# Kernel optimization log

Hardware: AMD Instinct MI355X
Metric: run time of the kernel (lower is better)

Reference implementation:

```python
import jax, jax.numpy as jnp
import numpy as np

B, C, H, W, L, R = 1, 32, 96, 128, 2, 3
N = 2 * R + 1
EPS = 1e-5


def conv2d(x, w, stride=1, pad=1):
    return jax.lax.conv_general_dilated(
        x, w, (stride, stride), ((pad, pad), (pad, pad)),
        dimension_numbers=('NCHW', 'OIHW', 'NCHW'))


def conv_transpose2d(x, w, stride=2, pad=1):
    # torch ConvTranspose2d semantics; w: [Cin, Cout, kH, kW]
    kh, kw = w.shape[2], w.shape[3]
    wf = jnp.flip(w, (2, 3)).transpose(1, 0, 2, 3)  # [Cout, Cin, kh, kw]
    return jax.lax.conv_general_dilated(
        x, wf, (1, 1),
        ((kh - 1 - pad, kh - 1 - pad), (kw - 1 - pad, kw - 1 - pad)),
        lhs_dilation=(stride, stride),
        dimension_numbers=('NCHW', 'OIHW', 'NCHW'))


def bnorm(x, s, b, m, v):
    # inference-mode BatchNorm2d (fixed running stats)
    inv = s * jax.lax.rsqrt(v + EPS)
    return x * inv[None, :, None, None] + (b - m * inv)[None, :, None, None]


def grid_sample(img, grid):
    # bilinear, align_corners=True, padding_mode='zeros'
    # img [B,C,H,W], grid [B,Hg,Wg,2] (x,y) in [-1,1]
    Bi, Ci, Hi, Wi = img.shape
    gx = (grid[..., 0] + 1.0) * 0.5 * (Wi - 1)
    gy = (grid[..., 1] + 1.0) * 0.5 * (Hi - 1)
    x0 = jnp.floor(gx)
    y0 = jnp.floor(gy)
    wx = (gx - x0)[:, None]  # [B,1,Hg,Wg]
    wy = (gy - y0)[:, None]

    def tap(yf, xf):
        valid = (xf >= 0) & (xf <= Wi - 1) & (yf >= 0) & (yf <= Hi - 1)
        xc = jnp.clip(xf, 0, Wi - 1).astype(jnp.int32)
        yc = jnp.clip(yf, 0, Hi - 1).astype(jnp.int32)
        v = jax.vmap(lambda im, y, x: im[:, y, x])(img, yc, xc)  # [B,C,Hg,Wg]
        return v * valid[:, None].astype(img.dtype)

    v00 = tap(y0, x0)
    v01 = tap(y0, x0 + 1)
    v10 = tap(y0 + 1, x0)
    v11 = tap(y0 + 1, x0 + 1)
    return (v00 * (1 - wx) * (1 - wy) + v01 * wx * (1 - wy)
            + v10 * (1 - wx) * wy + v11 * wx * wy)


def _forward(fmap1_0, fmap1_1, fmap2_0, fmap2_1, coords,
             cw1, cw2, cw3, cw4, ctw5, cw6, cb6,
             bn1s, bn1b, bn1m, bn1v, bn2s, bn2b, bn2m, bn2v,
             bn3s, bn3b, bn3m, bn3v, bn4s, bn4b, bn4m, bn4v,
             bn5s, bn5b, bn5m, bn5v, dap_w):
    n = N
    dx = jnp.linspace(-R, R, n)
    delta = jnp.stack(jnp.meshgrid(dx, dx, indexing='ij'), axis=-1)  # [n,n,2]
    b, _, h, w = coords.shape
    cp = coords.transpose(0, 2, 3, 1)  # [b,h,w,2] (x,y)
    bns = ((bn1s, bn1b, bn1m, bn1v), (bn2s, bn2b, bn2m, bn2v),
           (bn3s, bn3b, bn3m, bn3v), (bn4s, bn4b, bn4m, bn4v),
           (bn5s, bn5b, bn5m, bn5v))
    out = []
    for i, (f1, f2) in enumerate(((fmap1_0, fmap2_0), (fmap1_1, fmap2_1))):
        c, h2, w2 = f1.shape[1], f1.shape[2], f1.shape[3]
        # [b,n,h,n,w,2]: first n axis pairs with h, second with w (as in torch view)
        cent = cp[:, None, :, None, :, :] / (2.0 ** i) + delta[None, :, None, :, None, :]
        gx = 2.0 * cent[..., 0] / (w2 - 1) - 1.0
        gy = 2.0 * cent[..., 1] / (h2 - 1) - 1.0
        grid = jnp.stack([gx, gy], -1).reshape(b, n * h, n * w, 2)
        f2s = grid_sample(f2, grid).reshape(b, c, n, h, n, w)
        f2s = f2s.transpose(0, 2, 4, 1, 3, 5)  # [b,du,dv,c,h,w]
        f1e = jnp.broadcast_to(f1[:, None, None], (b, n, n, c, h, w))
        x = jnp.concatenate([f1e, f2s], axis=3).reshape(b * n * n, 2 * c, h, w)
        # MatchingNet (DICL): conv-bn-relu stack, stride-2 down + transposed up
        x = jax.nn.relu(bnorm(conv2d(x, cw1[i]), *(p[i] for p in bns[0])))
        x = jax.nn.relu(bnorm(conv2d(x, cw2[i], stride=2), *(p[i] for p in bns[1])))
        x = jax.nn.relu(bnorm(conv2d(x, cw3[i]), *(p[i] for p in bns[2])))
        x = jax.nn.relu(bnorm(conv2d(x, cw4[i]), *(p[i] for p in bns[3])))
        x = jax.nn.relu(bnorm(conv_transpose2d(x, ctw5[i]), *(p[i] for p in bns[4])))
        x = conv2d(x, cw6[i]) + cb6[i][None, :, None, None]  # [b*n*n,1,h,w]
        cost = x.reshape(b, n * n, h, w)
        # DisplacementAwareProjection: 1x1 conv over the 49 displacement channels
        cost = jnp.einsum('pq,bqhw->bphw', dap_w[i], cost)
        out.append(cost)
    return jnp.concatenate(out, axis=1)  # [b, L*(2r+1)^2, h, w]


def setup_inputs():
    key = jax.random.key(0)
    ks = jax.random.split(key, 40)

    def rn(k, shape, scale=1.0):
        return jax.random.normal(k, shape, jnp.float32) * scale

    inp = {}
    inp['fmap1_0'] = rn(ks[0], (B, C, H, W))
    inp['fmap2_0'] = rn(ks[1], (B, C, H, W))
    inp['fmap1_1'] = rn(ks[2], (B, C, H, W))
    inp['fmap2_1'] = rn(ks[3], (B, C, H, W))
    gy, gx = jnp.meshgrid(jnp.arange(H, dtype=jnp.float32),
                          jnp.arange(W, dtype=jnp.float32), indexing='ij')
    base = jnp.stack([gx, gy], 0)[None]  # [1,2,H,W] (x,y) pixel coords
    inp['coords'] = base + rn(ks[4], (B, 2, H, W), 2.0)

    def cw(k, co, ci, kk):
        return rn(k, (L, co, ci, kk, kk), 1.0 / np.sqrt(ci * kk * kk))

    inp['cw1'] = cw(ks[5], 96, 2 * C, 3)
    inp['cw2'] = cw(ks[6], 128, 96, 3)
    inp['cw3'] = cw(ks[7], 128, 128, 3)
    inp['cw4'] = cw(ks[8], 64, 128, 3)
    inp['ctw5'] = rn(ks[9], (L, 64, 32, 4, 4), 1.0 / np.sqrt(64 * 16))
    inp['cw6'] = cw(ks[10], 1, 32, 3)
    inp['cb6'] = rn(ks[11], (L, 1), 0.1)
    for j, ch in enumerate((96, 128, 128, 64, 32), start=1):
        k4 = jax.random.split(ks[11 + j], 4)
        inp['bn%ds' % j] = 1.0 + rn(k4[0], (L, ch), 0.1)
        inp['bn%db' % j] = rn(k4[1], (L, ch), 0.1)
        inp['bn%dm' % j] = rn(k4[2], (L, ch), 0.1)
        inp['bn%dv' % j] = 1.0 + rn(k4[3], (L, ch), 0.1) ** 2
    # DAP identity init
    inp['dap_w'] = jnp.tile(jnp.eye(N * N, dtype=jnp.float32)[None], (L, 1, 1))
    return inp


def reference(fmap1_0, fmap1_1, fmap2_0, fmap2_1, coords,
              cw1, cw2, cw3, cw4, ctw5, cw6, cb6,
              bn1s, bn1b, bn1m, bn1v, bn2s, bn2b, bn2m, bn2v,
              bn3s, bn3b, bn3m, bn3v, bn4s, bn4b, bn4m, bn4v,
              bn5s, bn5b, bn5m, bn5v, dap_w):
    return _forward(fmap1_0, fmap1_1, fmap2_0, fmap2_1, coords,
                    cw1, cw2, cw3, cw4, ctw5, cw6, cb6,
                    bn1s, bn1b, bn1m, bn1v, bn2s, bn2b, bn2m, bn2v,
                    bn3s, bn3b, bn3m, bn3v, bn4s, bn4b, bn4m, bn4v,
                    bn5s, bn5b, bn5m, bn5v, dap_w)
```

## Files before the change

### kernel.cpp

```cpp
#include <hip/hip_runtime.h>

#define EPSF 1e-5f

typedef __attribute__((ext_vector_type(8))) short short8;
typedef __attribute__((ext_vector_type(4))) float f32x4;

__device__ __forceinline__ ushort f2bf(float x) {
    union { float f; unsigned u; } c; c.f = x;
    unsigned r = c.u + 0x7FFF + ((c.u >> 16) & 1);
    return (ushort)(r >> 16);
}
__device__ __forceinline__ float bf2f(ushort b) {
    union { unsigned u; float f; } c; c.u = ((unsigned)b) << 16;
    return c.f;
}
__device__ __forceinline__ int swz(int a) {
    return a ^ (((a >> 7) & 7) << 4);
}


__global__ __launch_bounds__(256) void k_repack_conv(
    const float* __restrict__ src, ushort* __restrict__ dst, int CO, int CI)
{
    int idx = blockIdx.x * 256 + threadIdx.x;
    if (idx >= CO * CI * 9) return;
    int co = idx / (CI * 9);
    int rem = idx % (CI * 9);
    int ci = rem / 9, tap = rem % 9;
    dst[((size_t)tap * CO + co) * CI + ci] = f2bf(src[idx]);
}

__global__ __launch_bounds__(256) void k_repack_ct(
    const float* __restrict__ src, ushort* __restrict__ dst)
{
    int idx = blockIdx.x * 256 + threadIdx.x;
    if (idx >= 4 * 4 * 32 * 64) return;
    int ci = idx & 63;
    int t = idx >> 6;
    int co = t & 31; t >>= 5;
    int tap = t & 3;
    int parity = t >> 2;
    int ph = parity >> 1, pw = parity & 1;
    int a = tap >> 1, b = tap & 1;
    int kh = ((ph + 1) & 1) + 2 * a;
    int kw = ((pw + 1) & 1) + 2 * b;
    dst[idx] = f2bf(src[((ci * 32 + co) * 4 + kh) * 4 + kw]);
}

__global__ __launch_bounds__(256) void k_pack_f1(
    const float* __restrict__ f1_0, const float* __restrict__ f1_1,
    ushort* __restrict__ xf1)
{
    const int sp = blockIdx.x * 256 + threadIdx.x;
    const int l = blockIdx.z;
    const float* f1 = l ? f1_1 : f1_0;
    ushort* dst = xf1 + (size_t)l * 393216 + (size_t)sp * 32;
    #pragma unroll
    for (int g = 0; g < 4; ++g) {
        uint4 pk;
        uint* pw_ = (uint*)&pk;
        #pragma unroll
        for (int q = 0; q < 4; ++q) {
            int c = g * 8 + q * 2;
            pw_[q] = (uint)f2bf(f1[(size_t)c * 12288 + sp])
                   | ((uint)f2bf(f1[(size_t)(c + 1) * 12288 + sp]) << 16);
        }
        *(uint4*)(dst + g * 8) = pk;
    }
}

__global__ __launch_bounds__(256) void k_sample_nhwc(
    const float* __restrict__ f2_0, const float* __restrict__ f2_1,
    const float* __restrict__ coords, ushort* __restrict__ x0s, int d0)
{
    const int HW = 12288;
    const int sp = blockIdx.x * 256 + threadIdx.x;
    const int slot = blockIdx.z;
    const int p = d0 + slot;
    const int l = p / 49;
    const int d = p - l * 49;
    const int du = d / 7, dv = d % 7;
    const float inv_scale = l ? 0.5f : 1.0f;
    const float* f2 = l ? f2_1 : f2_0;

    float cx = coords[sp] * inv_scale + (float)(du - 3);
    float cy = coords[HW + sp] * inv_scale + (float)(dv - 3);
    float xf = floorf(cx), yf = floorf(cy);
    float wx = cx - xf, wy = cy - yf;
    int xi = (int)xf, yi = (int)yf;
    float vx0 = (xf >= 0.f && xf <= 127.f) ? 1.f : 0.f;
    float vx1 = (xf + 1.f >= 0.f && xf + 1.f <= 127.f) ? 1.f : 0.f;
    float vy0 = (yf >= 0.f && yf <= 95.f) ? 1.f : 0.f;
    float vy1 = (yf + 1.f >= 0.f && yf + 1.f <= 95.f) ? 1.f : 0.f;
    int x0i = min(max(xi, 0), 127), x1i = min(max(xi + 1, 0), 127);
    int y0i = min(max(yi, 0), 95),  y1i = min(max(yi + 1, 0), 95);
    float w00 = (1.f - wx) * (1.f - wy) * vx0 * vy0;
    float w01 = wx * (1.f - wy) * vx1 * vy0;
    float w10 = (1.f - wx) * wy * vx0 * vy1;
    float w11 = wx * wy * vx1 * vy1;
    int o00 = y0i * 128 + x0i, o01 = y0i * 128 + x1i;
    int o10 = y1i * 128 + x0i, o11 = y1i * 128 + x1i;

    ushort* dst = x0s + ((size_t)slot * HW + sp) * 32;
    #pragma unroll
    for (int g = 0; g < 4; ++g) {
        uint4 pk;
        uint* pw_ = (uint*)&pk;
        #pragma unroll
        for (int q = 0; q < 4; ++q) {
            uint wv = 0;
            #pragma unroll
            for (int h = 0; h < 2; ++h) {
                int c = g * 8 + q * 2 + h;
                const float* fc = f2 + (size_t)c * HW;
                float s = w00 * fc[o00] + w01 * fc[o01] + w10 * fc[o10] + w11 * fc[o11];
                wv |= ((uint)f2bf(s)) << (16 * h);
            }
            pw_[q] = wv;
        }
        *(uint4*)(dst + g * 8) = pk;
    }
}

template <int EPI>
__global__ __launch_bounds__(512, 2) void k_conv1(
    const ushort* __restrict__ in,
    ushort* __restrict__ out,
    const ushort* __restrict__ wbase,
    const float* __restrict__ p1,
    const float* __restrict__ bs0, const float* __restrict__ bb0,
    const float* __restrict__ bm0, const float* __restrict__ bv0,
    int d0, int koff)
{
    constexpr int AB = 10 * 66 * 64;
    constexpr int PB = 3 * 48 * 64;
    constexpr int SA = 6;
    __shared__ __align__(16) char smem[AB + 2 * PB];
    char* As = smem;

    const int tid = threadIdx.x;
    const int lane = tid & 63, wid = tid >> 6;
    const int lr = lane & 15, kg = lane >> 4;
    const int bx = blockIdx.x;
    const int rt = bx >> 1, ct = bx & 1;
    const int r0 = rt * 8, c0 = ct * 64;
    const int y = blockIdx.y;
    const int co0 = y * 48;
    const int slot = blockIdx.z;
    const int l = EPI ? slot : (d0 + slot) / 49;

    const ushort* ib = in + (size_t)slot * 12288 * 32;
    const ushort* wl = wbase + (size_t)l * (9 * 96 * 64);
    const short8 z8 = {0, 0, 0, 0, 0, 0, 0, 0};

    #pragma unroll
    for (int i = 0; i < SA; ++i) {
        int lin = i * 8192 + tid * 16;
        if (lin < AB) {
            int pos = lin >> 6;
            int prow = (pos * 994) >> 16;
            int pcol = pos - prow * 66;
            int grow = r0 - 1 + prow, gcol = c0 - 1 + pcol;
            bool ok = ((unsigned)grow < 96u) && ((unsigned)gcol < 128u);
            short8 v = z8;
            if (ok) v = *(const short8*)(ib + (grow * 128 + gcol) * 32 + ((lin & 63) >> 1));
            *(short8*)(As + swz(lin)) = v;
        }
    }

    int boff[2]; unsigned bmask = 0;
    #pragma unroll
    for (int i = 0; i < 2; ++i) {
        int lin = i * 8192 + tid * 16;
        if (lin < PB) bmask |= 1u << i;
        int lc = min(lin, PB - 16);
        int rowidx = lc >> 6;
        int tpg = rowidx / 48;
        int r = rowidx - tpg * 48;
        boff[i] = (tpg * 96 + co0 + r) * 64 + koff + ((lc & 63) >> 1);
    }
    short8 stgB[2];
    auto loadB = [&](int pg) {
        const ushort* src = wl + pg * (3 * 96 * 64);
        #pragma unroll
        for (int i = 0; i < 2; ++i)
            if ((bmask >> i) & 1) stgB[i] = *(const short8*)(src + boff[i]);
    };
    auto writeB = [&](int pg) {
        char* Bs = smem + AB + (pg & 1) * PB;
        #pragma unroll
        for (int i = 0; i < 2; ++i) {
            int lin = i * 8192 + tid * 16;
            if ((bmask >> i) & 1) *(short8*)(Bs + swz(lin)) = stgB[i];
        }
    };

    f32x4 acc[4][3];
    if constexpr (EPI == 0) {
        const float* pl = p1 + (size_t)l * 1179648
                        + ((size_t)((bx * 2 + y) * 512 + tid)) * 48;
        #pragma unroll
        for (int mf = 0; mf < 4; ++mf)
            #pragma unroll
            for (int nf = 0; nf < 3; ++nf)
                acc[mf][nf] = *(const f32x4*)(pl + (mf * 3 + nf) * 4);
    } else {
        #pragma unroll
        for (int mf = 0; mf < 4; ++mf)
            #pragma unroll
            for (int nf = 0; nf < 3; ++nf)
                acc[mf][nf] = (f32x4){0.f, 0.f, 0.f, 0.f};
    }

    loadB(0);
    writeB(0);
    __syncthreads();

    #pragma unroll
    for (int ps = 0; ps < 3; ++ps) {
        if (ps < 2) loadB(ps + 1);
        const char* Bs = smem + AB + (ps & 1) * PB;
        #pragma unroll
        for (int kw = 0; kw < 3; ++kw) {
            short8 a[4];
            #pragma unroll
            for (int mf = 0; mf < 4; ++mf) {
                int sp = (wid + ps) * 66 + mf * 16 + lr + kw;
                a[mf] = *(const short8*)(As + swz(sp * 64 + kg * 16));
            }
            #pragma unroll
            for (int nf = 0; nf < 3; ++nf) {
                short8 b = *(const short8*)(Bs + swz((kw * 48 + nf * 16 + lr) * 64 + kg * 16));
                #pragma unroll
                for (int mf = 0; mf < 4; ++mf)
                    acc[mf][nf] = __builtin_amdgcn_mfma_f32_16x16x32_bf16(
                        a[mf], b, acc[mf][nf], 0, 0, 0);
            }
        }
        __syncthreads();
        if (ps < 2) { writeB(ps + 1); __syncthreads(); }
    }

    if constexpr (EPI == 1) {
        float* of = (float*)out + (size_t)l * 1179648
                  + ((size_t)((bx * 2 + y) * 512 + tid)) * 48;
        #pragma unroll
        for (int mf = 0; mf < 4; ++mf)
            #pragma unroll
            for (int nf = 0; nf < 3; ++nf)
                *(f32x4*)(of + (mf * 3 + nf) * 4) = acc[mf][nf];
    } else {
        const float* bs = bs0 + l * 96;
        const float* bb = bb0 + l * 96;
        const float* bm = bm0 + l * 96;
        const float* bv = bv0 + l * 96;
        ushort* ob = out + (size_t)slot * 12288 * 96;
        const int orow = r0 + wid;
        #pragma unroll
        for (int nf = 0; nf < 3; ++nf) {
            const int col = co0 + nf * 16 + lr;
            const float inv = bs[col] * rsqrtf(bv[col] + EPSF);
            const float beta = bb[col] - bm[col] * inv;
            #pragma unroll
            for (int mf = 0; mf < 4; ++mf) {
                #pragma unroll
                for (int j = 0; j < 4; ++j) {
                    int ocol = c0 + mf * 16 + kg * 4 + j;
                    float yv = fmaxf(fmaf(acc[mf][nf][j], inv, beta), 0.f);
                    ob[((size_t)orow * 128 + ocol) * 96 + col] = f2bf(yv);
                }
            }
        }
    }
}

template <int CIN, int COUT, int ROWS, int IH, int IW>
__global__ __launch_bounds__(512) void k_conv_lds8(
    const ushort* __restrict__ in, ushort* __restrict__ out,
    const ushort* __restrict__ wbase, int wlstride,
    const float* __restrict__ bs0, const float* __restrict__ bb0,
    const float* __restrict__ bm0, const float* __restrict__ bv0, int d0)
{
    constexpr int NFT = ROWS / 16;
    constexpr int CC = CIN / 64;
    constexpr int NCT = IW / 64;
    constexpr int AB = 10 * 66 * 128;
    constexpr int PB = 3 * ROWS * 128;
    constexpr int SA = (AB + 8191) / 8192;
    constexpr int SB = (PB + 8191) / 8192;
    constexpr int NPH = 3 * CC;
    __shared__ __align__(16) char smem[AB + 2 * PB];
    char* As = smem;

    const int tid = threadIdx.x;
    const int lane = tid & 63, wid = tid >> 6;
    const int lr = lane & 15, kg = lane >> 4;
    const int rt = (int)blockIdx.x / NCT, ct = (int)blockIdx.x % NCT;
    const int r0 = rt * 8, c0 = ct * 64;
    const int co0 = blockIdx.y * ROWS;
    const int slot = blockIdx.z;
    const int l = (d0 + slot) / 49;

    int aoff[SA]; unsigned awr = 0, avalid = 0;
    #pragma unroll
    for (int i = 0; i < SA; ++i) {
        int lin = i * 8192 + tid * 16;
        bool wr = lin < AB;
        int linc = wr ? lin : 0;
        int pos = linc >> 7;
        int prow = (pos * 994) >> 16;
        int pcol = pos - prow * 66;
        int grow = r0 - 1 + prow, gcol = c0 - 1 + pcol;
        bool ok = wr && ((unsigned)grow < (unsigned)IH) && ((unsigned)gcol < (unsigned)IW);
        if (wr) awr |= 1u << i;
        if (ok) avalid |= 1u << i;
        int growc = min(max(grow, 0), IH - 1), gcolc = min(max(gcol, 0), IW - 1);
        aoff[i] = (growc * IW + gcolc) * CIN + ((linc & 127) >> 1);
    }
    int boff[SB]; unsigned bmask = 0;
    #pragma unroll
    for (int i = 0; i < SB; ++i) {
        int lin = i * 8192 + tid * 16;
        if (lin < PB) bmask |= 1u << i;
        int lc = min(lin, PB - 16);
        int rowidx = lc >> 7;
        int tpg = rowidx / ROWS, r = rowidx - tpg * ROWS;
        boff[i] = (tpg * COUT + co0 + r) * CIN + ((lc & 127) >> 1);
    }

    const ushort* ib = in + (size_t)slot * IH * IW * CIN;
    const ushort* wl = wbase + (size_t)l * wlstride;
    const short8 z8 = {0, 0, 0, 0, 0, 0, 0, 0};

    short8 stgA[SA], stgB[SB];
    auto loadA = [&](int cc) {
        #pragma unroll
        for (int i = 0; i < SA; ++i) {
            if ((avalid >> i) & 1) stgA[i] = *(const short8*)(ib + aoff[i] + cc * 64);
            else stgA[i] = z8;
        }
    };
    auto writeA = [&]() {
        #pragma unroll
        for (int i = 0; i < SA; ++i) {
            int lin = i * 8192 + tid * 16;
            if ((awr >> i) & 1)
                *(short8*)(As + swz(lin)) = stgA[i];
        }
    };
    auto loadB = [&](int ps) {
        int pg = ps % 3, cc = ps / 3;
        const ushort* src = wl + pg * (3 * COUT * CIN) + cc * 64;
        #pragma unroll
        for (int i = 0; i < SB; ++i)
            if ((bmask >> i) & 1) stgB[i] = *(const short8*)(src + boff[i]);
    };
    auto writeB = [&](int ps) {
        char* Bs = smem + AB + (ps & 1) * PB;
        #pragma unroll
        for (int i = 0; i < SB; ++i) {
            int lin = i * 8192 + tid * 16;
            if ((bmask >> i) & 1)
                *(short8*)(Bs + swz(lin)) = stgB[i];
        }
    };

    f32x4 acc[4][NFT];
    #pragma unroll
    for (int mf = 0; mf < 4; ++mf)
        #pragma unroll
        for (int nf = 0; nf < NFT; ++nf)
            acc[mf][nf] = (f32x4){0.f, 0.f, 0.f, 0.f};

    loadA(0); loadB(0);
    writeA(); writeB(0);
    __syncthreads();

    #pragma unroll 1
    for (int ps = 0; ps < NPH; ++ps) {
        const int pg = ps % 3;
        const bool hasNext = (ps + 1 < NPH);
        const bool newA = (CC > 1) && (pg == 2) && hasNext;
        if (hasNext) loadB(ps + 1);
        if (newA) loadA(ps / 3 + 1);

        const char* Bs = smem + AB + (ps & 1) * PB;
        #pragma unroll
        for (int kw = 0; kw < 3; ++kw) {
            const int spb = (wid + pg) * 66 + lr + kw;
            #pragma unroll
            for (int ks = 0; ks < 2; ++ks) {
                short8 a[4];
                #pragma unroll
                for (int mf = 0; mf < 4; ++mf) {
                    int sp = spb + mf * 16;
                    a[mf] = *(const short8*)(As + swz(sp * 128 + ks * 64 + kg * 16));
                }
                #pragma unroll
                for (int nf = 0; nf < NFT; ++nf) {
                    int rb = kw * ROWS + nf * 16 + lr;
                    short8 b = *(const short8*)(Bs + swz(rb * 128 + ks * 64 + kg * 16));
                    #pragma unroll
                    for (int mf = 0; mf < 4; ++mf)
                        acc[mf][nf] = __builtin_amdgcn_mfma_f32_16x16x32_bf16(
                            a[mf], b, acc[mf][nf], 0, 0, 0);
                }
            }
        }

        __syncthreads();
        if (hasNext) writeB(ps + 1);
        if (newA) writeA();
        if (hasNext) __syncthreads();
    }

    const float* bs = bs0 + l * COUT;
    const float* bb = bb0 + l * COUT;
    const float* bm = bm0 + l * COUT;
    const float* bv = bv0 + l * COUT;
    ushort* ob = out + (size_t)slot * IH * IW * COUT;
    const int orow = r0 + wid;
    #pragma unroll
    for (int nf = 0; nf < NFT; ++nf) {
        const int col = co0 + nf * 16 + lr;
        const float inv = bs[col] * rsqrtf(bv[col] + EPSF);
        const float beta = bb[col] - bm[col] * inv;
        #pragma unroll
        for (int mf = 0; mf < 4; ++mf) {
            #pragma unroll
            for (int j = 0; j < 4; ++j) {
                int ocol = c0 + mf * 16 + kg * 4 + j;
                float y = fmaxf(fmaf(acc[mf][nf][j], inv, beta), 0.f);
                ob[((size_t)orow * IW + ocol) * COUT + col] = f2bf(y);
            }
        }
    }
}

__global__ __launch_bounds__(512, 2) void k_conv_s2_8(
    const ushort* __restrict__ in, ushort* __restrict__ out,
    const ushort* __restrict__ wbase, int wlstride,
    const float* __restrict__ bs0, const float* __restrict__ bb0,
    const float* __restrict__ bm0, const float* __restrict__ bv0, int d0)
{
    constexpr int AB = 9 * 66 * 64;
    constexpr int PB = 3 * 64 * 64;
    constexpr int SA = 5;
    constexpr int SB = 2;
    constexpr int NPH = 9;
    __shared__ __align__(16) char smem[AB + 2 * PB];
    char* As = smem;

    const int tid = threadIdx.x;
    const int lane = tid & 63, wid = tid >> 6;
    const int lr = lane & 15, kg = lane >> 4;
    const int mw = wid >> 1, ch = wid & 1;
    const int bx = blockIdx.x;
    const int rt = bx >> 1, ct = bx & 1;
    const int r0 = rt * 4, oc0 = ct * 32;
    const int co0 = blockIdx.y * 64;
    const int slot = blockIdx.z;
    const int l = (d0 + slot) / 49;

    int aoff[SA]; unsigned awr = 0, avalid = 0;
    #pragma unroll
    for (int i = 0; i < SA; ++i) {
        int lin = i * 8192 + tid * 16;
        bool wr = lin < AB;
        int linc = wr ? lin : 0;
        int pos = linc >> 6;
        int prow = (pos * 994) >> 16;
        int pcol = pos - prow * 66;
        int grow = 2 * r0 - 1 + prow, gcol = 2 * oc0 - 1 + pcol;
        bool ok = wr && ((unsigned)grow < 96u) && ((unsigned)gcol < 128u);
        if (wr) awr |= 1u << i;
        if (ok) avalid |= 1u << i;
        int growc = min(max(grow, 0), 95), gcolc = min(max(gcol, 0), 127);
        aoff[i] = (growc * 128 + gcolc) * 96 + ((linc & 63) >> 1);
    }
    int boff[SB]; unsigned bmask = 0;
    #pragma unroll
    for (int i = 0; i < SB; ++i) {
        int lin = i * 8192 + tid * 16;
        if (lin < PB) bmask |= 1u << i;
        int lc = min(lin, PB - 16);
        int rowidx = lc >> 6;
        int tpg = rowidx >> 6, r = rowidx & 63;
        boff[i] = (tpg * 128 + co0 + r) * 96 + ((lc & 63) >> 1);
    }

    const ushort* ib = in + (size_t)slot * 12288 * 96;
    const ushort* wl = wbase + (size_t)l * wlstride;
    const short8 z8 = {0, 0, 0, 0, 0, 0, 0, 0};

    short8 stgA[SA], stgB[SB];
    auto loadA = [&](int cc) {
        #pragma unroll
        for (int i = 0; i < SA; ++i) {
            if ((avalid >> i) & 1) stgA[i] = *(const short8*)(ib + aoff[i] + cc * 32);
            else stgA[i] = z8;
        }
    };
    auto writeA = [&]() {
        #pragma unroll
        for (int i = 0; i < SA; ++i) {
            int lin = i * 8192 + tid * 16;
            if ((awr >> i) & 1)
                *(short8*)(As + swz(lin)) = stgA[i];
        }
    };
    auto loadB = [&](int ps) {
        int pg = ps % 3, cc = ps / 3;
        const ushort* src = wl + pg * (3 * 128 * 96) + cc * 32;
        #pragma unroll
        for (int i = 0; i < SB; ++i)
            if ((bmask >> i) & 1) stgB[i] = *(const short8*)(src + boff[i]);
    };
    auto writeB = [&](int ps) {
        char* Bs = smem + AB + (ps & 1) * PB;
        #pragma unroll
        for (int i = 0; i < SB; ++i) {
            int lin = i * 8192 + tid * 16;
            if ((bmask >> i) & 1)
                *(short8*)(Bs + swz(lin)) = stgB[i];
        }
    };

    f32x4 acc[2][2];
    #pragma unroll
    for (int mf = 0; mf < 2; ++mf)
        #pragma unroll
        for (int nf = 0; nf < 2; ++nf)
            acc[mf][nf] = (f32x4){0.f, 0.f, 0.f, 0.f};

    loadA(0); loadB(0);
    writeA(); writeB(0);
    __syncthreads();

    #pragma unroll 1
    for (int ps = 0; ps < NPH; ++ps) {
        const int pg = ps % 3;
        const bool hasNext = (ps + 1 < NPH);
        const bool newA = (pg == 2) && hasNext;
        if (hasNext) loadB(ps + 1);
        if (newA) loadA(ps / 3 + 1);

        const char* Bs = smem + AB + (ps & 1) * PB;
        #pragma unroll
        for (int kw = 0; kw < 3; ++kw) {
            short8 a[2];
            #pragma unroll
            for (int mf = 0; mf < 2; ++mf) {
                int pos = (2 * mw + pg) * 66 + 2 * (mf * 16 + lr) + kw;
                a[mf] = *(const short8*)(As + swz(pos * 64 + kg * 16));
            }
            #pragma unroll
            for (int nf = 0; nf < 2; ++nf) {
                int rb = kw * 64 + ch * 32 + nf * 16 + lr;
                short8 b = *(const short8*)(Bs + swz(rb * 64 + kg * 16));
                #pragma unroll
                for (int mf = 0; mf < 2; ++mf)
                    acc[mf][nf] = __builtin_amdgcn_mfma_f32_16x16x32_bf16(
                        a[mf], b, acc[mf][nf], 0, 0, 0);
            }
        }

        __syncthreads();
        if (hasNext) writeB(ps + 1);
        if (newA) writeA();
        if (hasNext) __syncthreads();
    }

    const float* bs = bs0 + l * 128;
    const float* bb = bb0 + l * 128;
    const float* bm = bm0 + l * 128;
    const float* bv = bv0 + l * 128;
    ushort* ob = out + (size_t)slot * 3072 * 128;
    const int orow = r0 + mw;
    #pragma unroll
    for (int nf = 0; nf < 2; ++nf) {
        const int col = co0 + ch * 32 + nf * 16 + lr;
        const float inv = bs[col] * rsqrtf(bv[col] + EPSF);
        const float beta = bb[col] - bm[col] * inv;
        #pragma unroll
        for (int mf = 0; mf < 2; ++mf) {
            #pragma unroll
            for (int j = 0; j < 4; ++j) {
                int ocol = oc0 + mf * 16 + kg * 4 + j;
                float y = fmaxf(fmaf(acc[mf][nf][j], inv, beta), 0.f);
                ob[((size_t)orow * 64 + ocol) * 128 + col] = f2bf(y);
            }
        }
    }
}

__global__ __launch_bounds__(256) void k_convt_mfma(
    const ushort* __restrict__ in, ushort* __restrict__ out,
    const ushort* __restrict__ wbase,
    const float* __restrict__ bs0, const float* __restrict__ bb0,
    const float* __restrict__ bm0, const float* __restrict__ bv0, int d0)
{
    constexpr int SLICE = 4 * 32 * 128;
    constexpr int S = 4;
    __shared__ __align__(16) char smem[SLICE];

    const int tid = threadIdx.x;
    const int lane = tid & 63, wid = tid >> 6;
    const int lr = lane & 15, kg = lane >> 4;
    const int m0 = blockIdx.x * 256 + wid * 64;
    const int parity = blockIdx.y;
    const int slot = blockIdx.z;
    const int l = (d0 + slot) / 49;
    const int ph = parity >> 1, pw = parity & 1;
    const int kh0 = (ph + 1) & 1, kw0 = (pw + 1) & 1;

    {
        const char* wsrc = (const char*)(wbase + (size_t)l * (16 * 32 * 64));
        #pragma unroll
        for (int i = 0; i < S; ++i) {
            int lin = i * 4096 + tid * 16;
            int rowidx = lin >> 7;
            int tap = rowidx >> 5, r = rowidx & 31;
            short8 v = *(const short8*)(wsrc
                + (((size_t)(parity * 4 + tap) * 32 + r) * 64) * 2 + (lin & 127));
            *(short8*)(smem + swz(lin)) = v;
        }
    }
    __syncthreads();

    int ihA[4], iwA[4];
    #pragma unroll
    for (int mf = 0; mf < 4; ++mf) {
        int m = m0 + mf * 16 + lr;
        int q = m >> 6, r = m & 63;
        ihA[mf] = (2 * q + ph + 1 - kh0) >> 1;
        iwA[mf] = (2 * r + pw + 1 - kw0) >> 1;
    }
    const ushort* ib = in + (size_t)slot * 3072 * 64;

    const short8 z8 = {0, 0, 0, 0, 0, 0, 0, 0};
    f32x4 acc[4][2];
    #pragma unroll
    for (int mf = 0; mf < 4; ++mf)
        #pragma unroll
        for (int nf = 0; nf < 2; ++nf)
            acc[mf][nf] = (f32x4){0.f, 0.f, 0.f, 0.f};

    #pragma unroll
    for (int a = 0; a < 2; ++a) {
        #pragma unroll
        for (int b2 = 0; b2 < 2; ++b2) {
            int srcoff[4]; bool val[4];
            #pragma unroll
            for (int mf = 0; mf < 4; ++mf) {
                int ih = ihA[mf] - a;
                int iw = iwA[mf] - b2;
                val[mf] = ((unsigned)ih < 48u) && ((unsigned)iw < 64u);
                int ihc = min(max(ih, 0), 47), iwc = min(max(iw, 0), 63);
                srcoff[mf] = (ihc * 64 + iwc) * 64;
            }
            const int tap = a * 2 + b2;
            #pragma unroll
            for (int cc = 0; cc < 2; ++cc) {
                const int kbase = cc * 32 + kg * 8;
                short8 av[4];
                #pragma unroll
                for (int mf = 0; mf < 4; ++mf) {
                    short8 v = *(const short8*)(ib + srcoff[mf] + kbase);
                    av[mf] = val[mf] ? v : z8;
                }
                #pragma unroll
                for (int nf = 0; nf < 2; ++nf) {
                    short8 bfr = *(const short8*)(smem
                        + swz((tap * 32 + nf * 16 + lr) * 128 + cc * 64 + kg * 16));
                    #pragma unroll
                    for (int mf = 0; mf < 4; ++mf)
                        acc[mf][nf] = __builtin_amdgcn_mfma_f32_16x16x32_bf16(
                            av[mf], bfr, acc[mf][nf], 0, 0, 0);
                }
            }
        }
    }

    const float* bs = bs0 + l * 32;
    const float* bb = bb0 + l * 32;
    const float* bm = bm0 + l * 32;
    const float* bv = bv0 + l * 32;
    ushort* ob = out + (size_t)slot * 12288 * 32;
    #pragma unroll
    for (int nf = 0; nf < 2; ++nf) {
        const int col = nf * 16 + lr;
        const float inv = bs[col] * rsqrtf(bv[col] + EPSF);
        const float beta = bb[col] - bm[col] * inv;
        #pragma unroll
        for (int mf = 0; mf < 4; ++mf) {
            #pragma unroll
            for (int j = 0; j < 4; ++j) {
                int m = m0 + mf * 16 + kg * 4 + j;
                int q = m >> 6, r = m & 63;
                int sp = (2 * q + ph) * 128 + (2 * r + pw);
                float y = fmaxf(fmaf(acc[mf][nf][j], inv, beta), 0.f);
                ob[(size_t)sp * 32 + col] = f2bf(y);
            }
        }
    }
}

__global__ __launch_bounds__(256) void k_conv6(
    const ushort* __restrict__ x5, float* __restrict__ cost,
    const float* __restrict__ w0, const float* __restrict__ cb6, int d0)
{
    const int sp = blockIdx.x * 256 + threadIdx.x;
    const int slot = blockIdx.z;
    const int p = d0 + slot;
    const int l = p / 49;
    const float* w = w0 + l * 288;
    const int oh = sp >> 7, ow = sp & 127;
    float acc = 0.f;
    #pragma unroll
    for (int kh = 0; kh < 3; ++kh) {
        const int ih = oh - 1 + kh;
        if (ih < 0 || ih >= 96) continue;
        #pragma unroll
        for (int kw = 0; kw < 3; ++kw) {
            const int iw = ow - 1 + kw;
            if (iw < 0 || iw >= 128) continue;
            const ushort* q = x5 + ((size_t)slot * 12288 + ih * 128 + iw) * 32;
            const int tap = kh * 3 + kw;
            #pragma unroll
            for (int g = 0; g < 4; ++g) {
                uint4 v = *(const uint4*)(q + g * 8);
                const uint* vw = (const uint*)&v;
                #pragma unroll
                for (int t = 0; t < 4; ++t) {
                    int ci = g * 8 + t * 2;
                    acc = fmaf(bf2f((ushort)(vw[t] & 0xFFFF)), w[ci * 9 + tap], acc);
                    acc = fmaf(bf2f((ushort)(vw[t] >> 16)), w[(ci + 1) * 9 + tap], acc);
                }
            }
        }
    }
    cost[(size_t)p * 12288 + sp] = acc + cb6[l];
}

__global__ __launch_bounds__(256) void k_dap(
    const float* __restrict__ cost, const float* __restrict__ dw,
    float* __restrict__ out)
{
    const int sp = blockIdx.x * 256 + threadIdx.x;
    const int p = blockIdx.y;
    const float* dr = dw + p * 49;
    float acc = 0.f;
    #pragma unroll
    for (int q = 0; q < 49; ++q)
        acc = fmaf(dr[q], cost[(size_t)q * 12288 + sp], acc);
    out[(size_t)p * 12288 + sp] = acc;
}

extern "C" void kernel_launch(void* const* d_in, const int* in_sizes, int n_in,
                              void* d_out, int out_size, void* d_ws, size_t ws_size,
                              hipStream_t stream)
{
    const float* fm1_0 = (const float*)d_in[0];
    const float* fm2_0 = (const float*)d_in[1];
    const float* fm1_1 = (const float*)d_in[2];
    const float* fm2_1 = (const float*)d_in[3];
    const float* coords = (const float*)d_in[4];
    const float* cw1  = (const float*)d_in[5];
    const float* cw2  = (const float*)d_in[6];
    const float* cw3  = (const float*)d_in[7];
    const float* cw4  = (const float*)d_in[8];
    const float* ctw5 = (const float*)d_in[9];
    const float* cw6  = (const float*)d_in[10];
    const float* cb6  = (const float*)d_in[11];
    const float* bn[5][4];
    for (int j = 0; j < 5; ++j)
        for (int k = 0; k < 4; ++k)
            bn[j][k] = (const float*)d_in[12 + j * 4 + k];
    const float* dap = (const float*)d_in[32];
    float* out = (float*)d_out;

    const size_t A_US = 393216;
    const size_t B_US = 1179648;
    const size_t XF1 = 2 * 393216;
    const size_t W1 = 9 * 96 * 64, W2 = 9 * 128 * 96, W3 = 9 * 128 * 128;
    const size_t W4 = 9 * 64 * 128, W5 = 16 * 32 * 64;
    const size_t W_US = 2 * (W1 + W2 + W3 + W4 + W5);
    const size_t P1F = 2 * (size_t)24 * 2 * 512 * 48;
    const size_t COSTF = (size_t)98 * 12288;

    int DC = 1;
    for (int cand : {98, 66, 49, 42, 33, 25, 17, 13, 9, 7, 5, 3, 2, 1}) {
        size_t need = (A_US + B_US) * (size_t)cand * 2 + (XF1 + W_US) * 2
                    + (P1F + COSTF) * 4 + 4096;
        if (need <= ws_size) { DC = cand; break; }
    }

    ushort* bufA = (ushort*)d_ws;
    ushort* bufB = bufA + A_US * DC;
    ushort* xf1 = bufB + B_US * DC;
    ushort* wp = xf1 + XF1;
    ushort* wr1 = wp; wp += 2 * W1;
    ushort* wr2 = wp; wp += 2 * W2;
    ushort* wr3 = wp; wp += 2 * W3;
    ushort* wr4 = wp; wp += 2 * W4;
    ushort* wr5 = wp; wp += 2 * W5;
    float* P1 = (float*)wp;
    float* cost = P1 + P1F;

    for (int l = 0; l < 2; ++l) {
        k_repack_conv<<<dim3(216), 256, 0, stream>>>(cw1 + (size_t)l * W1, wr1 + l * W1, 96, 64);
        k_repack_conv<<<dim3(432), 256, 0, stream>>>(cw2 + (size_t)l * W2, wr2 + l * W2, 128, 96);
        k_repack_conv<<<dim3(576), 256, 0, stream>>>(cw3 + (size_t)l * W3, wr3 + l * W3, 128, 128);
        k_repack_conv<<<dim3(288), 256, 0, stream>>>(cw4 + (size_t)l * W4, wr4 + l * W4, 64, 128);
        k_repack_ct<<<dim3(128), 256, 0, stream>>>(ctw5 + (size_t)l * W5, wr5 + l * W5);
    }

    k_pack_f1<<<dim3(48, 1, 2), 256, 0, stream>>>(fm1_0, fm1_1, xf1);
    k_conv1<1><<<dim3(24, 2, 2), 512, 0, stream>>>(
        xf1, (ushort*)P1, wr1, nullptr,
        bn[0][0], bn[0][1], bn[0][2], bn[0][3], 0, 0);

    for (int d0 = 0; d0 < 98; d0 += DC) {
        const int ndd = min(DC, 98 - d0);
        k_sample_nhwc<<<dim3(48, 1, ndd), 256, 0, stream>>>(
            fm2_0, fm2_1, coords, bufA, d0);
        k_conv1<0><<<dim3(24, 2, ndd), 512, 0, stream>>>(
            bufA, bufB, wr1, P1,
            bn[0][0], bn[0][1], bn[0][2], bn[0][3], d0, 32);
        k_conv_s2_8<<<dim3(24, 2, ndd), 512, 0, stream>>>(bufB, bufA, wr2, (int)W2,
                bn[1][0], bn[1][1], bn[1][2], bn[1][3], d0);
        k_conv_lds8<128, 128, 64, 48, 64>
            <<<dim3(6, 2, ndd), 512, 0, stream>>>(bufA, bufB, wr3, (int)W3,
                bn[2][0], bn[2][1], bn[2][2], bn[2][3], d0);
        k_conv_lds8<128, 64, 64, 48, 64>
            <<<dim3(6, 1, ndd), 512, 0, stream>>>(bufB, bufA, wr4, (int)W4,
                bn[3][0], bn[3][1], bn[3][2], bn[3][3], d0);
        k_convt_mfma<<<dim3(12, 4, ndd), 256, 0, stream>>>(bufA, bufB, wr5,
                bn[4][0], bn[4][1], bn[4][2], bn[4][3], d0);
        k_conv6<<<dim3(48, 1, ndd), 256, 0, stream>>>(
            bufB, cost, cw6, cb6, d0);
    }
    for (int l = 0; l < 2; ++l)
        k_dap<<<dim3(48, 49), 256, 0, stream>>>(
            cost + (size_t)l * 49 * 12288, dap + (size_t)l * 49 * 49,
            out + (size_t)l * 49 * 12288);
}
```

Before: 746.5 us.

## Shrink conv LDS tiles to 32-channel K-chunks for higher occupancy

Rewrites the 3x3 conv kernels for layers 3 and 4 to stage 32 input channels per phase instead of 64. The A and B LDS tiles are halved, so the kernel requests four 512-thread blocks per CU through launch_bounds. The A tile is now loaded directly into LDS when needed rather than prefetched into registers, which cuts register pressure. The cost is twice as many phases and barriers, and the A loads are no longer overlapped with compute.

```diff
diff --git a/kernel.cpp b/kernel.cpp
--- a/kernel.cpp
+++ b/kernel.cpp
@@ -274,30 +274,26 @@
     }
 }
 
-template <int CIN, int COUT, int ROWS, int IH, int IW>
-__global__ __launch_bounds__(512) void k_conv_lds8(
+template <int CIN, int COUT, int IH, int IW>
+__global__ __launch_bounds__(512, 4) void k_conv_lds8s(
     const ushort* __restrict__ in, ushort* __restrict__ out,
     const ushort* __restrict__ wbase, int wlstride,
     const float* __restrict__ bs0, const float* __restrict__ bb0,
     const float* __restrict__ bm0, const float* __restrict__ bv0, int d0)
 {
-    constexpr int NFT = ROWS / 16;
-    constexpr int CC = CIN / 64;
-    constexpr int NCT = IW / 64;
-    constexpr int AB = 10 * 66 * 128;
-    constexpr int PB = 3 * ROWS * 128;
-    constexpr int SA = (AB + 8191) / 8192;
-    constexpr int SB = (PB + 8191) / 8192;
-    constexpr int NPH = 3 * CC;
+    constexpr int CCs = CIN / 32;
+    constexpr int AB = 10 * 66 * 64;
+    constexpr int PB = 3 * 64 * 64;
+    constexpr int SA = 6, SB = 2;
+    constexpr int NPH = 3 * CCs;
     __shared__ __align__(16) char smem[AB + 2 * PB];
     char* As = smem;
 
     const int tid = threadIdx.x;
     const int lane = tid & 63, wid = tid >> 6;
     const int lr = lane & 15, kg = lane >> 4;
-    const int rt = (int)blockIdx.x / NCT, ct = (int)blockIdx.x % NCT;
-    const int r0 = rt * 8, c0 = ct * 64;
-    const int co0 = blockIdx.y * ROWS;
+    const int r0 = (int)blockIdx.x * 8;
+    const int co0 = (int)blockIdx.y * 64;
     const int slot = blockIdx.z;
     const int l = (d0 + slot) / 49;
 
@@ -307,15 +303,15 @@
         int lin = i * 8192 + tid * 16;
         bool wr = lin < AB;
         int linc = wr ? lin : 0;
-        int pos = linc >> 7;
+        int pos = linc >> 6;
         int prow = (pos * 994) >> 16;
         int pcol = pos - prow * 66;
-        int grow = r0 - 1 + prow, gcol = c0 - 1 + pcol;
+        int grow = r0 - 1 + prow, gcol = pcol - 1;
         bool ok = wr && ((unsigned)grow < (unsigned)IH) && ((unsigned)gcol < (unsigned)IW);
         if (wr) awr |= 1u << i;
         if (ok) avalid |= 1u << i;
         int growc = min(max(grow, 0), IH - 1), gcolc = min(max(gcol, 0), IW - 1);
-        aoff[i] = (growc * IW + gcolc) * CIN + ((linc & 127) >> 1);
+        aoff[i] = (growc * IW + gcolc) * CIN + ((linc & 63) >> 1);
     }
     int boff[SB]; unsigned bmask = 0;
     #pragma unroll
@@ -323,34 +319,31 @@
         int lin = i * 8192 + tid * 16;
         if (lin < PB) bmask |= 1u << i;
         int lc = min(lin, PB - 16);
-        int rowidx = lc >> 7;
-        int tpg = rowidx / ROWS, r = rowidx - tpg * ROWS;
-        boff[i] = (tpg * COUT + co0 + r) * CIN + ((lc & 127) >> 1);
+        int rowidx = lc >> 6;
+        int tpg = rowidx >> 6, r = rowidx & 63;
+        boff[i] = (tpg * COUT + co0 + r) * CIN + ((lc & 63) >> 1);
     }
 
     const ushort* ib = in + (size_t)slot * IH * IW * CIN;
     const ushort* wl = wbase + (size_t)l * wlstride;
     const short8 z8 = {0, 0, 0, 0, 0, 0, 0, 0};
 
-    short8 stgA[SA], stgB[SB];
-    auto loadA = [&](int cc) {
-        #pragma unroll
-        for (int i = 0; i < SA; ++i) {
-            if ((avalid >> i) & 1) stgA[i] = *(const short8*)(ib + aoff[i] + cc * 64);
-            else stgA[i] = z8;
-        }
-    };
-    auto writeA = [&]() {
+    auto stageA = [&](int cc) {
         #pragma unroll
         for (int i = 0; i < SA; ++i) {
             int lin = i * 8192 + tid * 16;
-            if ((awr >> i) & 1)
-                *(short8*)(As + swz(lin)) = stgA[i];
+            if ((awr >> i) & 1) {
+                short8 v = z8;
+                if ((avalid >> i) & 1)
+                    v = *(const short8*)(ib + aoff[i] + cc * 32);
+                *(short8*)(As + swz(lin)) = v;
+            }
         }
     };
+    short8 stgB[SB];
     auto loadB = [&](int ps) {
         int pg = ps % 3, cc = ps / 3;
-        const ushort* src = wl + pg * (3 * COUT * CIN) + cc * 64;
+        const ushort* src = wl + pg * (3 * COUT * CIN) + cc * 32;
         #pragma unroll
         for (int i = 0; i < SB; ++i)
             if ((bmask >> i) & 1) stgB[i] = *(const short8*)(src + boff[i]);
@@ -360,58 +353,52 @@
         #pragma unroll
         for (int i = 0; i < SB; ++i) {
             int lin = i * 8192 + tid * 16;
-            if ((bmask >> i) & 1)
-                *(short8*)(Bs + swz(lin)) = stgB[i];
+            if ((bmask >> i) & 1) *(short8*)(Bs + swz(lin)) = stgB[i];
         }
     };
 
-    f32x4 acc[4][NFT];
+    f32x4 acc[4][4];
     #pragma unroll
     for (int mf = 0; mf < 4; ++mf)
         #pragma unroll
-        for (int nf = 0; nf < NFT; ++nf)
+        for (int nf = 0; nf < 4; ++nf)
             acc[mf][nf] = (f32x4){0.f, 0.f, 0.f, 0.f};
 
-    loadA(0); loadB(0);
-    writeA(); writeB(0);
+    stageA(0);
+    loadB(0); writeB(0);
     __syncthreads();
 
     #pragma unroll 1
     for (int ps = 0; ps < NPH; ++ps) {
         const int pg = ps % 3;
         const bool hasNext = (ps + 1 < NPH);
-        const bool newA = (CC > 1) && (pg == 2) && hasNext;
         if (hasNext) loadB(ps + 1);
-        if (newA) loadA(ps / 3 + 1);
 
         const char* Bs = smem + AB + (ps & 1) * PB;
         #pragma unroll
         for (int kw = 0; kw < 3; ++kw) {
-            const int spb = (wid + pg) * 66 + lr + kw;
-            #pragma unroll
-            for (int ks = 0; ks < 2; ++ks) {
-                short8 a[4];
+            short8 a[4];
+            #pragma unroll
+            for (int mf = 0; mf < 4; ++mf) {
+                int sp = (wid + pg) * 66 + mf * 16 + lr + kw;
+                a[mf] = *(const short8*)(As + swz(sp * 64 + kg * 16));
+            }
+            #pragma unroll
+            for (int nf = 0; nf < 4; ++nf) {
+                short8 b = *(const short8*)(Bs + swz((kw * 64 + nf * 16 + lr) * 64 + kg * 16));
                 #pragma unroll
-                for (int mf = 0; mf < 4; ++mf) {
-                    int sp = spb + mf * 16;
-                    a[mf] = *(const short8*)(As + swz(sp * 128 + ks * 64 + kg * 16));
-                }
-                #pragma unroll
-                for (int nf = 0; nf < NFT; ++nf) {
-                    int rb = kw * ROWS + nf * 16 + lr;
-                    short8 b = *(const short8*)(Bs + swz(rb * 128 + ks * 64 + kg * 16));
-                    #pragma unroll
-                    for (int mf = 0; mf < 4; ++mf)
-                        acc[mf][nf] = __builtin_amdgcn_mfma_f32_16x16x32_bf16(
-                            a[mf], b, acc[mf][nf], 0, 0, 0);
-                }
+                for (int mf = 0; mf < 4; ++mf)
+                    acc[mf][nf] = __builtin_amdgcn_mfma_f32_16x16x32_bf16(
+                        a[mf], b, acc[mf][nf], 0, 0, 0);
             }
         }
 
         __syncthreads();
-        if (hasNext) writeB(ps + 1);
-        if (newA) writeA();
-        if (hasNext) __syncthreads();
+        if (hasNext) {
+            writeB(ps + 1);
+            if (pg == 2) stageA(ps / 3 + 1);
+            __syncthreads();
+        }
     }
 
     const float* bs = bs0 + l * COUT;
@@ -421,7 +408,7 @@
     ushort* ob = out + (size_t)slot * IH * IW * COUT;
     const int orow = r0 + wid;
     #pragma unroll
-    for (int nf = 0; nf < NFT; ++nf) {
+    for (int nf = 0; nf < 4; ++nf) {
         const int col = co0 + nf * 16 + lr;
         const float inv = bs[col] * rsqrtf(bv[col] + EPSF);
         const float beta = bb[col] - bm[col] * inv;
@@ -429,7 +416,7 @@
         for (int mf = 0; mf < 4; ++mf) {
             #pragma unroll
             for (int j = 0; j < 4; ++j) {
-                int ocol = c0 + mf * 16 + kg * 4 + j;
+                int ocol = mf * 16 + kg * 4 + j;
                 float y = fmaxf(fmaf(acc[mf][nf][j], inv, beta), 0.f);
                 ob[((size_t)orow * IW + ocol) * COUT + col] = f2bf(y);
             }
@@ -830,10 +817,10 @@
             bn[0][0], bn[0][1], bn[0][2], bn[0][3], d0, 32);
         k_conv_s2_8<<<dim3(24, 2, ndd), 512, 0, stream>>>(bufB, bufA, wr2, (int)W2,
                 bn[1][0], bn[1][1], bn[1][2], bn[1][3], d0);
-        k_conv_lds8<128, 128, 64, 48, 64>
+        k_conv_lds8s<128, 128, 48, 64>
             <<<dim3(6, 2, ndd), 512, 0, stream>>>(bufA, bufB, wr3, (int)W3,
                 bn[2][0], bn[2][1], bn[2][2], bn[2][3], d0);
-        k_conv_lds8<128, 64, 64, 48, 64>
+        k_conv_lds8s<128, 64, 48, 64>
             <<<dim3(6, 1, ndd), 512, 0, stream>>>(bufB, bufA, wr4, (int)W4,
                 bn[3][0], bn[3][1], bn[3][2], bn[3][3], d0);
         k_convt_mfma<<<dim3(12, 4, ndd), 256, 0, stream>>>(bufA, bufB, wr5,
```

Measured after the change: 753.4 us. Within noise of the previous version (+0.9%).
